# Kernel optimization log

Measured on AMD Instinct MI355X. Metric: run time of the kernel, lower is better.

## Reference

```python
import jax, jax.numpy as jnp
import numpy as np


def setup_inputs() -> dict:
    key = jax.random.key(0)
    ks = jax.random.split(key, 6)
    B, T, U = 4, 160, 80
    De, Dd = 640, 640
    inner, vocab = 640, 1024
    return {
        "enc_state": jax.random.normal(ks[0], (B, T, De), jnp.float32),
        "dec_state": jax.random.normal(ks[1], (B, U, Dd), jnp.float32),
        "W1": jax.random.normal(ks[2], (De + Dd, inner), jnp.float32) * (1.0 / np.sqrt(De + Dd)),
        "b1": jax.random.normal(ks[3], (inner,), jnp.float32) * 0.02,
        "W2": jax.random.normal(ks[4], (inner, vocab), jnp.float32) * (1.0 / np.sqrt(inner)),
        "b2": jax.random.normal(ks[5], (vocab,), jnp.float32) * 0.02,
    }


def reference(enc_state, dec_state, W1, b1, W2, b2):
    # Faithful to: cat([enc tiled over U, dec tiled over T], -1) @ W1 + b1,
    # algebraically split so the [B,T,U,2D] concat is never materialized:
    # cat(e, d) @ W1 == e @ W1[:De] + d @ W1[De:]
    De = enc_state.shape[-1]
    W1_enc, W1_dec = W1[:De], W1[De:]
    enc_proj = jnp.einsum("btd,dh->bth", enc_state, W1_enc)   # [B,T,H]
    dec_proj = jnp.einsum("bud,dh->buh", dec_state, W1_dec)   # [B,U,H]
    # broadcast add over the (T,U) lattice -> [B,T,U,H]
    hidden = jnp.tanh(enc_proj[:, :, None, :] + dec_proj[:, None, :, :] + b1)
    logits = jnp.einsum("btuh,hv->btuv", hidden, W2) + b2     # [B,T,U,V]
    return logits
```

## Files before the change

### kernel.cpp

```cpp
#include <hip/hip_runtime.h>
#include <hip/hip_bf16.h>
#include <cstdint>

#define D_    640
#define V_    1024
#define M_    51200

typedef __bf16 bf16x8 __attribute__((ext_vector_type(8)));
typedef float floatx4 __attribute__((ext_vector_type(4)));

__device__ __forceinline__ void g2l16(const void* g, void* l) {
    __builtin_amdgcn_global_load_lds((const __attribute__((address_space(1))) void*)g,
                                     (__attribute__((address_space(3))) void*)l,
                                     16, 0, 0);
}

__device__ __forceinline__ float fast_tanh(float x) {
    float e = __builtin_amdgcn_exp2f(x * 2.8853900817779268f);
    return 1.0f - 2.0f * __builtin_amdgcn_rcpf(e + 1.0f);
}

__global__ __launch_bounds__(256) void proj_kernel(
    const float* __restrict__ enc, const float* __restrict__ dec,
    const float* __restrict__ W1, const float* __restrict__ b1,
    float* __restrict__ encp, float* __restrict__ decp) {
    __shared__ float As[64][36];
    __shared__ float Ws[32][68];

    const int rt = blockIdx.y;
    const int ct = blockIdx.x;
    const bool is_enc = (rt < 10);
    const float* Asrc; const float* Wsrc; float* Cdst;
    if (is_enc) { Asrc = enc + (size_t)rt * 64 * D_;        Wsrc = W1;           Cdst = encp + (size_t)rt * 64 * D_; }
    else        { Asrc = dec + (size_t)(rt - 10) * 64 * D_; Wsrc = W1 + D_ * D_; Cdst = decp + (size_t)(rt - 10) * 64 * D_; }

    const int tid = threadIdx.x;
    const int ar = tid >> 2,  ac = (tid & 3) * 8;
    const int wr2 = tid >> 3, wc2 = (tid & 7) * 8;
    const int tr = tid >> 4,  tc = tid & 15;

    float acc[4][4] = {};
    for (int k0 = 0; k0 < D_; k0 += 32) {
        __syncthreads();
        *(floatx4*)&As[ar][ac]       = *(const floatx4*)&Asrc[(size_t)ar * D_ + k0 + ac];
        *(floatx4*)&As[ar][ac + 4]   = *(const floatx4*)&Asrc[(size_t)ar * D_ + k0 + ac + 4];
        *(floatx4*)&Ws[wr2][wc2]     = *(const floatx4*)&Wsrc[(size_t)(k0 + wr2) * D_ + ct * 64 + wc2];
        *(floatx4*)&Ws[wr2][wc2 + 4] = *(const floatx4*)&Wsrc[(size_t)(k0 + wr2) * D_ + ct * 64 + wc2 + 4];
        __syncthreads();
#pragma unroll
        for (int kk = 0; kk < 32; kk++) {
            floatx4 w = *(const floatx4*)&Ws[kk][tc * 4];
            float a0 = As[tr * 4 + 0][kk], a1 = As[tr * 4 + 1][kk];
            float a2 = As[tr * 4 + 2][kk], a3 = As[tr * 4 + 3][kk];
#pragma unroll
            for (int j = 0; j < 4; j++) {
                acc[0][j] += a0 * w[j]; acc[1][j] += a1 * w[j];
                acc[2][j] += a2 * w[j]; acc[3][j] += a3 * w[j];
            }
        }
    }
    floatx4 bv = {0.f, 0.f, 0.f, 0.f};
    if (is_enc) bv = *(const floatx4*)&b1[ct * 64 + tc * 4];
#pragma unroll
    for (int i = 0; i < 4; i++) {
        floatx4 v = { acc[i][0] + bv[0], acc[i][1] + bv[1],
                      acc[i][2] + bv[2], acc[i][3] + bv[3] };
        *(floatx4*)&Cdst[(size_t)(tr * 4 + i) * D_ + ct * 64 + tc * 4] = v;
    }
}

__global__ __launch_bounds__(256) void w2t_kernel(
    const float* __restrict__ W2, __bf16* __restrict__ W2t) {
    __shared__ __bf16 tile[32][33];
    const int vt = blockIdx.x;
    const int kt = blockIdx.y;
    const int tx = threadIdx.x & 31, ty = threadIdx.x >> 5;
#pragma unroll
    for (int i = 0; i < 4; i++)
        tile[ty + i * 8][tx] = (__bf16)W2[(size_t)(kt * 32 + ty + i * 8) * V_ + vt * 32 + tx];
    __syncthreads();
#pragma unroll
    for (int i = 0; i < 4; i++)
        W2t[(size_t)(vt * 32 + ty + i * 8) * D_ + kt * 32 + tx] = tile[tx][ty + i * 8];
}

__global__ __launch_bounds__(256, 2) void joint_kernel(
    const float* __restrict__ encp, const float* __restrict__ decp,
    const __bf16* __restrict__ W2t, const float* __restrict__ b2,
    float* __restrict__ C) {
    __shared__ __align__(128) char lds[81920];

    const int bid = blockIdx.x;
    const int swz = (bid & 7) * 400 + (bid >> 3);
    const int mt = swz >> 2, nt = swz & 3;
    const int m0 = mt * 64, n0 = nt * 256;

    const int tid = threadIdx.x;
    const int w = tid >> 6, l = tid & 63;
    const int lr = l & 15, lk = l >> 4;

    char* ldsp = (char*)lds;

    const char* Wb = (const char*)W2t
        + (size_t)(n0 + (tid >> 3)) * 1280
        + (unsigned)((((tid & 7) ^ ((tid >> 3) & 7)) * 16));
    const unsigned bdst = 16384u + (unsigned)tid * 16u;

    const int pr = tid >> 2;
    const int kq = tid & 3;
    const int R  = m0 + pr;
    const int bt = R / 80;
    const int uu = R - bt * 80;
    const int drw = (bt / 160) * 80 + uu;
    const float* ep = encp + (size_t)bt * D_ + kq * 16;
    const float* dp = decp + (size_t)drw * D_ + kq * 16;
    const unsigned pw0 = (unsigned)(pr * 128 + (((kq * 2)     ^ (pr & 7)) * 16));
    const unsigned pw1 = (unsigned)(pr * 128 + (((kq * 2 + 1) ^ (pr & 7)) * 16));

    floatx4 acc[4][4] = {};

#define STAGE_B(BUF, T) do { \
    const char* _s = Wb + (size_t)(T) * 128; \
    char* _d = ldsp + bdst + (BUF) * 32768; \
    g2l16(_s,           _d); \
    g2l16(_s +  40960,  _d +  4096); \
    g2l16(_s +  81920,  _d +  8192); \
    g2l16(_s + 122880,  _d + 12288); \
    g2l16(_s + 163840,  _d + 16384); \
    g2l16(_s + 204800,  _d + 20480); \
    g2l16(_s + 245760,  _d + 24576); \
    g2l16(_s + 286720,  _d + 28672); \
  } while (0)

#define LOAD_ED(T) do { \
    const float* _e = ep + (T) * 64; const float* _d = dp + (T) * 64; \
    _Pragma("unroll") for (int q = 0; q < 4; ++q) { \
      eD[q] = *(const floatx4*)(_e + q * 4); \
      dD[q] = *(const floatx4*)(_d + q * 4); \
    } } while (0)

#define PRODUCE_A(BUF) do { \
    bf16x8 h0, h1; \
    _Pragma("unroll") for (int q = 0; q < 4; ++q) { \
      _Pragma("unroll") for (int i2 = 0; i2 < 4; ++i2) { \
        float t_ = fast_tanh(eD[q][i2] + dD[q][i2]); \
        if (q < 2) h0[q * 4 + i2] = (__bf16)t_; else h1[(q - 2) * 4 + i2] = (__bf16)t_; \
      } } \
    *(bf16x8*)(ldsp + (BUF) * 8192 + pw0) = h0; \
    *(bf16x8*)(ldsp + (BUF) * 8192 + pw1) = h1; \
  } while (0)

    {
        floatx4 eD[4], dD[4];
        STAGE_B(0, 0);
        LOAD_ED(0);
        PRODUCE_A(0);
    }
    __syncthreads();

#pragma unroll 1
    for (int t = 0; t < 10; ++t) {
        const int buf = t & 1, nb = buf ^ 1;
        floatx4 eD[4], dD[4];
        if (t < 9) {
            STAGE_B(nb, t + 1);
            LOAD_ED(t + 1);
        }
#pragma unroll
        for (int s = 0; s < 2; ++s) {
            const unsigned sx = (unsigned)((((s * 4 + lk) ^ (lr & 7)) * 16));
            bf16x8 af[4], bfr[4];
#pragma unroll
            for (int i = 0; i < 4; ++i)
                af[i] = *(const bf16x8*)(ldsp + buf * 8192 + (i * 16 + lr) * 128 + sx);
#pragma unroll
            for (int j = 0; j < 4; ++j)
                bfr[j] = *(const bf16x8*)(ldsp + 16384 + buf * 32768 + (w * 64 + j * 16 + lr) * 128 + sx);
#pragma unroll
            for (int i = 0; i < 4; ++i)
#pragma unroll
                for (int j = 0; j < 4; ++j)
                    acc[i][j] = __builtin_amdgcn_mfma_f32_16x16x32_bf16(af[i], bfr[j], acc[i][j], 0, 0, 0);
        }
        if (t < 9) {
            PRODUCE_A(nb);
        }
        __syncthreads();
    }

#pragma unroll
    for (int j = 0; j < 4; ++j) {
        const int col = n0 + w * 64 + j * 16 + lr;
        const float bj = b2[col];
#pragma unroll
        for (int i = 0; i < 4; ++i) {
            const int row = m0 + i * 16 + lk * 4;
            float* Cp = C + (size_t)row * V_ + col;
#pragma unroll
            for (int rg = 0; rg < 4; ++rg)
                Cp[(size_t)rg * V_] = acc[i][j][rg] + bj;
        }
    }
#undef STAGE_B
#undef LOAD_ED
#undef PRODUCE_A
}

extern "C" void kernel_launch(void* const* d_in, const int* in_sizes, int n_in,
                              void* d_out, int out_size, void* d_ws, size_t ws_size,
                              hipStream_t stream) {
    const float* enc = (const float*)d_in[0];
    const float* dec = (const float*)d_in[1];
    const float* W1  = (const float*)d_in[2];
    const float* b1  = (const float*)d_in[3];
    const float* W2  = (const float*)d_in[4];
    const float* b2  = (const float*)d_in[5];
    float* out = (float*)d_out;

    char* ws = (char*)d_ws;
    float*  encp = (float*)ws;
    float*  decp = (float*)(ws + 1638400);
    __bf16* W2t  = (__bf16*)(ws + 1638400 + 819200);

    proj_kernel<<<dim3(10, 15), 256, 0, stream>>>(enc, dec, W1, b1, encp, decp);
    w2t_kernel<<<dim3(32, 20), 256, 0, stream>>>(W2, W2t);
    joint_kernel<<<3200, 256, 0, stream>>>(encp, decp, W2t, b2, out);
}
```

Before: 334.7 us.

## Prefetch enc/dec rows two tiles ahead and use partial vmcnt barriers

```diff
diff --git a/kernel.cpp b/kernel.cpp
--- a/kernel.cpp
+++ b/kernel.cpp
@@ -83,6 +83,8 @@
     for (int i = 0; i < 4; i++)
         W2t[(size_t)(vt * 32 + ty + i * 8) * D_ + kt * 32 + tx] = tile[tx][ty + i * 8];
 }
+
+#define SCB  __builtin_amdgcn_sched_barrier(0)
 
 __global__ __launch_bounds__(256, 2) void joint_kernel(
     const float* __restrict__ encp, const float* __restrict__ decp,
@@ -132,61 +134,70 @@
     g2l16(_s + 286720,  _d + 28672); \
   } while (0)
 
-#define LOAD_ED(T) do { \
+#define LOAD_ED2(T, EV, DV) do { \
     const float* _e = ep + (T) * 64; const float* _d = dp + (T) * 64; \
     _Pragma("unroll") for (int q = 0; q < 4; ++q) { \
-      eD[q] = *(const floatx4*)(_e + q * 4); \
-      dD[q] = *(const floatx4*)(_d + q * 4); \
+      EV[q] = *(const floatx4*)(_e + q * 4); \
+      DV[q] = *(const floatx4*)(_d + q * 4); \
     } } while (0)
 
-#define PRODUCE_A(BUF) do { \
+#define PRODUCE_A2(BUF, EV, DV) do { \
     bf16x8 h0, h1; \
     _Pragma("unroll") for (int q = 0; q < 4; ++q) { \
       _Pragma("unroll") for (int i2 = 0; i2 < 4; ++i2) { \
-        float t_ = fast_tanh(eD[q][i2] + dD[q][i2]); \
+        float t_ = fast_tanh(EV[q][i2] + DV[q][i2]); \
         if (q < 2) h0[q * 4 + i2] = (__bf16)t_; else h1[(q - 2) * 4 + i2] = (__bf16)t_; \
       } } \
     *(bf16x8*)(ldsp + (BUF) * 8192 + pw0) = h0; \
     *(bf16x8*)(ldsp + (BUF) * 8192 + pw1) = h1; \
   } while (0)
 
+#define FRAGS_MFMA(BUF) do { \
+    _Pragma("unroll") \
+    for (int s = 0; s < 2; ++s) { \
+        const unsigned sx = (unsigned)((((s * 4 + lk) ^ (lr & 7)) * 16)); \
+        bf16x8 af[4], bfr[4]; \
+        _Pragma("unroll") for (int i = 0; i < 4; ++i) \
+            af[i] = *(const bf16x8*)(ldsp + (BUF) * 8192 + (i * 16 + lr) * 128 + sx); \
+        _Pragma("unroll") for (int j = 0; j < 4; ++j) \
+            bfr[j] = *(const bf16x8*)(ldsp + 16384 + (BUF) * 32768 + (w * 64 + j * 16 + lr) * 128 + sx); \
+        _Pragma("unroll") for (int i = 0; i < 4; ++i) \
+            _Pragma("unroll") for (int j = 0; j < 4; ++j) \
+                acc[i][j] = __builtin_amdgcn_mfma_f32_16x16x32_bf16(af[i], bfr[j], acc[i][j], 0, 0, 0); \
+    } } while (0)
+
+    floatx4 eC[4] = {}, dC[4] = {}, eN[4] = {}, dN[4] = {};
+
+    STAGE_B(0, 0);
+    SCB;
     {
-        floatx4 eD[4], dD[4];
-        STAGE_B(0, 0);
-        LOAD_ED(0);
-        PRODUCE_A(0);
-    }
-    __syncthreads();
+        floatx4 e0[4], d0[4];
+        LOAD_ED2(0, e0, d0);
+        LOAD_ED2(1, eC, dC);
+        PRODUCE_A2(0, e0, d0);
+    }
+    SCB;
+    asm volatile("s_waitcnt vmcnt(8) lgkmcnt(0)" ::: "memory");
+    __builtin_amdgcn_s_barrier();
+    SCB;
 
 #pragma unroll 1
-    for (int t = 0; t < 10; ++t) {
+    for (int t = 0; t < 9; ++t) {
         const int buf = t & 1, nb = buf ^ 1;
-        floatx4 eD[4], dD[4];
-        if (t < 9) {
-            STAGE_B(nb, t + 1);
-            LOAD_ED(t + 1);
-        }
-#pragma unroll
-        for (int s = 0; s < 2; ++s) {
-            const unsigned sx = (unsigned)((((s * 4 + lk) ^ (lr & 7)) * 16));
-            bf16x8 af[4], bfr[4];
-#pragma unroll
-            for (int i = 0; i < 4; ++i)
-                af[i] = *(const bf16x8*)(ldsp + buf * 8192 + (i * 16 + lr) * 128 + sx);
-#pragma unroll
-            for (int j = 0; j < 4; ++j)
-                bfr[j] = *(const bf16x8*)(ldsp + 16384 + buf * 32768 + (w * 64 + j * 16 + lr) * 128 + sx);
-#pragma unroll
-            for (int i = 0; i < 4; ++i)
-#pragma unroll
-                for (int j = 0; j < 4; ++j)
-                    acc[i][j] = __builtin_amdgcn_mfma_f32_16x16x32_bf16(af[i], bfr[j], acc[i][j], 0, 0, 0);
-        }
-        if (t < 9) {
-            PRODUCE_A(nb);
-        }
-        __syncthreads();
-    }
+        STAGE_B(nb, t + 1);
+        SCB;
+        if (t < 8) LOAD_ED2(t + 2, eN, dN);
+        FRAGS_MFMA(buf);
+        PRODUCE_A2(nb, eC, dC);
+#pragma unroll
+        for (int q = 0; q < 4; ++q) { eC[q] = eN[q]; dC[q] = dN[q]; }
+        SCB;
+        if (t == 8) { asm volatile("s_waitcnt vmcnt(0) lgkmcnt(0)" ::: "memory"); }
+        else        { asm volatile("s_waitcnt vmcnt(8) lgkmcnt(0)" ::: "memory"); }
+        __builtin_amdgcn_s_barrier();
+        SCB;
+    }
+    FRAGS_MFMA(1);
 
 #pragma unroll
     for (int j = 0; j < 4; ++j) {
@@ -202,8 +213,9 @@
         }
     }
 #undef STAGE_B
-#undef LOAD_ED
-#undef PRODUCE_A
+#undef LOAD_ED2
+#undef PRODUCE_A2
+#undef FRAGS_MFMA
 }
 
 extern "C" void kernel_launch(void* const* d_in, const int* in_sizes, int n_in,
```

Result: no change. 331.4 us, median of 2 (-1.0%).
